# Kernel tuning notes

Hardware: AMD Instinct MI355X
Metric: run time of the kernel (lower is better)

Reference implementation:

```python
import jax, jax.numpy as jnp
from jax import lax
import numpy as np

VOCAB, EMB, HID, B, T = 500, 64, 64, 512, 512


def setup_inputs() -> dict:
    key = jax.random.key(0)
    ks = jax.random.split(key, 12)
    s_ih = 1.0 / np.sqrt(HID)
    emb = jax.random.normal(ks[0], (VOCAB, EMB), dtype=jnp.float32)
    emb = emb.at[0].set(0.0)  # padding_idx=0 row is zero-initialized
    u = lambda k, shape: jax.random.uniform(k, shape, jnp.float32, -s_ih, s_ih)
    return {
        "x": jax.random.randint(ks[1], (B, T), 0, VOCAB, dtype=jnp.int64),
        "emb": emb,
        "W_ih0": u(ks[2], (HID, EMB)), "W_hh0": u(ks[3], (HID, HID)),
        "b_ih0": u(ks[4], (HID,)),     "b_hh0": u(ks[5], (HID,)),
        "W_ih1": u(ks[6], (HID, HID)), "W_hh1": u(ks[7], (HID, HID)),
        "b_ih1": u(ks[8], (HID,)),     "b_hh1": u(ks[9], (HID,)),
        "fc_w": u(ks[10], (1, HID)),   "fc_b": u(ks[11], (1,)),
    }


def reference(x, emb, W_ih0, W_hh0, b_ih0, b_hh0, W_ih1, W_hh1, b_ih1, b_hh1, fc_w, fc_b):
    e = emb[x]                                        # [B,T,EMB]
    # Layer-0 input projection is time-parallel; precompute as one big GEMM.
    xin0 = jnp.einsum('bte,he->bth', e, W_ih0) + b_ih0  # [B,T,HID]

    def step(carry, xt):
        h1, h2 = carry
        h1 = jnp.tanh(xt + h1 @ W_hh0.T + b_hh0)
        h2 = jnp.tanh(h1 @ W_ih1.T + b_ih1 + h2 @ W_hh1.T + b_hh1)
        return (h1, h2), None

    h0 = jnp.zeros((x.shape[0], HID), dtype=e.dtype)
    (h1, h2), _ = lax.scan(step, (h0, h0), jnp.swapaxes(xin0, 0, 1))  # scan over T
    return h2 @ fc_w.T + fc_b                          # [B,1]
```

## Files before the change

### kernel.cpp

```cpp
#include <hip/hip_runtime.h>
#include <math.h>

#define VOCAB 500
#define EMB   64
#define HID   64
#define BB    512
#define TT    512
#define KC    8
#define NC    (TT / KC)

__device__ __forceinline__ float fast_tanh(float x) {
    float ax = fabsf(x);
    float e  = __expf(-2.0f * ax);
    float r  = __builtin_amdgcn_rcpf(1.0f + e);
    float t  = fmaf(-2.0f * e, r, 1.0f);
    return copysignf(t, x);
}

__device__ __forceinline__ float bcast(float v, int lane) {
    return __int_as_float(__builtin_amdgcn_readlane(__float_as_int(v), lane));
}

__global__ __launch_bounds__(64) void proj_kernel(
        const float* __restrict__ emb,
        const float* __restrict__ W_ih0,
        const float* __restrict__ b_ih0,
        float* __restrict__ proj) {
    const int v = blockIdx.x;
    const int j = threadIdx.x;
    const float4* e4 = (const float4*)(emb + v * EMB);
    const float4* w4 = (const float4*)(W_ih0 + j * EMB);
    float acc = b_ih0[j];
    #pragma unroll
    for (int k = 0; k < EMB / 4; ++k) {
        float4 e = e4[k];
        float4 w = w4[k];
        acc = fmaf(w.x, e.x, acc);
        acc = fmaf(w.y, e.y, acc);
        acc = fmaf(w.z, e.z, acc);
        acc = fmaf(w.w, e.w, acc);
    }
    proj[v * HID + j] = acc;
}

__global__ __launch_bounds__(192, 1) void rnn_kernel(
        const int*   __restrict__ x,
        const float* __restrict__ proj,
        const float* __restrict__ W_hh0,
        const float* __restrict__ b_hh0,
        const float* __restrict__ W_ih1,
        const float* __restrict__ W_hh1,
        const float* __restrict__ b_ih1,
        const float* __restrict__ b_hh1,
        const float* __restrict__ fc_w,
        const float* __restrict__ fc_b,
        float* __restrict__ out) {
    const int b   = blockIdx.x;
    const int tid = threadIdx.x;
    const int wid = tid >> 6;
    const int j   = tid & 63;

    __shared__ __align__(16) float H1R[2][KC][HID];
    __shared__ __align__(16) float AAR[2][KC][HID];
    __shared__ int xls[TT];

    for (int t = tid; t < TT; t += 192) xls[t] = x[b * TT + t];

    const float* wsrc = (wid == 0 ? W_hh0 : (wid == 1 ? W_ih1 : W_hh1)) + j * HID;
    float w[HID];
    {
        const float4* w4 = (const float4*)wsrc;
        #pragma unroll
        for (int k = 0; k < HID / 4; ++k) {
            float4 t4 = w4[k];
            w[4*k+0] = t4.x; w[4*k+1] = t4.y; w[4*k+2] = t4.z; w[4*k+3] = t4.w;
        }
    }
    #pragma unroll
    for (int k = 0; k < HID; ++k) asm volatile("" : "+v"(w[k]));

    const float bh0 = b_hh0[j];
    const float bi1 = b_ih1[j] + b_hh1[j];
    const float fcw = fc_w[j];

    __syncthreads();

    float h1reg = 0.0f, h2reg = 0.0f;
    float xin[KC], xinN[KC];
    if (wid == 0) {
        #pragma unroll
        for (int u = 0; u < KC; ++u) xin[u] = proj[xls[u] * HID + j];
    }

    for (int c = 0; c < NC + 2; ++c) {
        if (wid == 0) {
            if (c < NC) {
                const int base = ((c + 1) & (NC - 1)) * KC;
                #pragma unroll
                for (int u = 0; u < KC; ++u)
                    xinN[u] = proj[xls[base + u] * HID + j];

                #pragma unroll
                for (int u = 0; u < KC; ++u) {
                    float a0 = xin[u] + bh0, a1 = 0.0f, a2 = 0.0f, a3 = 0.0f;
                    #pragma unroll
                    for (int k = 0; k < HID; k += 4) {
                        a0 = fmaf(w[k+0], bcast(h1reg, k+0), a0);
                        a1 = fmaf(w[k+1], bcast(h1reg, k+1), a1);
                        a2 = fmaf(w[k+2], bcast(h1reg, k+2), a2);
                        a3 = fmaf(w[k+3], bcast(h1reg, k+3), a3);
                    }
                    h1reg = fast_tanh((a0 + a1) + (a2 + a3));
                    H1R[c & 1][u][j] = h1reg;
                    xin[u] = xinN[u];
                }
            }
        } else if (wid == 1) {
            if (c >= 1 && c <= NC) {
                const int p = (c - 1) & 1;
                #pragma unroll
                for (int u = 0; u < KC; ++u) {
                    const float4* hv = (const float4*)(&H1R[p][u][0]);
                    float a0 = 0.0f, a1 = 0.0f, a2 = 0.0f, a3 = 0.0f;
                    #pragma unroll
                    for (int k = 0; k < HID / 4; ++k) {
                        float4 h = hv[k];
                        a0 = fmaf(w[4*k+0], h.x, a0);
                        a1 = fmaf(w[4*k+1], h.y, a1);
                        a2 = fmaf(w[4*k+2], h.z, a2);
                        a3 = fmaf(w[4*k+3], h.w, a3);
                    }
                    AAR[p][u][j] = (a0 + a1) + (a2 + a3);
                }
            }
        } else {
            if (c >= 2) {
                const int p = c & 1;
                #pragma unroll
                for (int u = 0; u < KC; ++u) {
                    float a0 = AAR[p][u][j] + bi1, a1 = 0.0f, a2 = 0.0f, a3 = 0.0f;
                    #pragma unroll
                    for (int k = 0; k < HID; k += 4) {
                        a0 = fmaf(w[k+0], bcast(h2reg, k+0), a0);
                        a1 = fmaf(w[k+1], bcast(h2reg, k+1), a1);
                        a2 = fmaf(w[k+2], bcast(h2reg, k+2), a2);
                        a3 = fmaf(w[k+3], bcast(h2reg, k+3), a3);
                    }
                    h2reg = fast_tanh((a0 + a1) + (a2 + a3));
                }
            }
        }
        __syncthreads();
    }

    if (wid == 2) {
        float val = h2reg * fcw;
        #pragma unroll
        for (int o = 32; o > 0; o >>= 1) val += __shfl_down(val, o, 64);
        if (j == 0) out[b] = val + fc_b[0];
    }
}

extern "C" void kernel_launch(void* const* d_in, const int* in_sizes, int n_in,
                              void* d_out, int out_size, void* d_ws, size_t ws_size,
                              hipStream_t stream) {
    const int*   x     = (const int*)  d_in[0];
    const float* emb   = (const float*)d_in[1];
    const float* W_ih0 = (const float*)d_in[2];
    const float* W_hh0 = (const float*)d_in[3];
    const float* b_ih0 = (const float*)d_in[4];
    const float* b_hh0 = (const float*)d_in[5];
    const float* W_ih1 = (const float*)d_in[6];
    const float* W_hh1 = (const float*)d_in[7];
    const float* b_ih1 = (const float*)d_in[8];
    const float* b_hh1 = (const float*)d_in[9];
    const float* fc_w  = (const float*)d_in[10];
    const float* fc_b  = (const float*)d_in[11];
    float* out  = (float*)d_out;
    float* proj = (float*)d_ws;

    proj_kernel<<<VOCAB, 64, 0, stream>>>(emb, W_ih0, b_ih0, proj);
    rnn_kernel<<<BB, 192, 0, stream>>>(x, proj, W_hh0, b_hh0,
                                       W_ih1, W_hh1, b_ih1, b_hh1,
                                       fc_w, fc_b, out);
}
```

Baseline: 318.4 us.

## Process two batch rows per block to interleave independent recurrences

```diff
diff --git a/kernel.cpp b/kernel.cpp
--- a/kernel.cpp
+++ b/kernel.cpp
@@ -6,7 +6,8 @@
 #define HID   64
 #define BB    512
 #define TT    512
-#define KC    8
+#define RB    2
+#define KC    4
 #define NC    (TT / KC)
 
 __device__ __forceinline__ float fast_tanh(float x) {
@@ -55,16 +56,17 @@
         const float* __restrict__ fc_w,
         const float* __restrict__ fc_b,
         float* __restrict__ out) {
-    const int b   = blockIdx.x;
+    const int b0  = blockIdx.x * RB;
     const int tid = threadIdx.x;
     const int wid = tid >> 6;
     const int j   = tid & 63;
 
-    __shared__ __align__(16) float H1R[2][KC][HID];
-    __shared__ __align__(16) float AAR[2][KC][HID];
-    __shared__ int xls[TT];
-
-    for (int t = tid; t < TT; t += 192) xls[t] = x[b * TT + t];
+    __shared__ __align__(16) float H1R[2][KC][RB][HID];
+    __shared__ __align__(16) float AAR[2][KC][RB][HID];
+    __shared__ int xls[RB][TT];
+
+    for (int t = tid; t < RB * TT; t += 192)
+        ((int*)xls)[t] = x[b0 * TT + t];
 
     const float* wsrc = (wid == 0 ? W_hh0 : (wid == 1 ? W_ih1 : W_hh1)) + j * HID;
     float w[HID];
@@ -85,11 +87,14 @@
 
     __syncthreads();
 
-    float h1reg = 0.0f, h2reg = 0.0f;
-    float xin[KC], xinN[KC];
+    float h1A = 0.0f, h1B = 0.0f, h2A = 0.0f, h2B = 0.0f;
+    float xinA[KC], xinB[KC], xnA[KC], xnB[KC];
     if (wid == 0) {
         #pragma unroll
-        for (int u = 0; u < KC; ++u) xin[u] = proj[xls[u] * HID + j];
+        for (int u = 0; u < KC; ++u) {
+            xinA[u] = proj[xls[0][u] * HID + j];
+            xinB[u] = proj[xls[1][u] * HID + j];
+        }
     }
 
     for (int c = 0; c < NC + 2; ++c) {
@@ -97,22 +102,31 @@
             if (c < NC) {
                 const int base = ((c + 1) & (NC - 1)) * KC;
                 #pragma unroll
-                for (int u = 0; u < KC; ++u)
-                    xinN[u] = proj[xls[base + u] * HID + j];
-
-                #pragma unroll
-                for (int u = 0; u < KC; ++u) {
-                    float a0 = xin[u] + bh0, a1 = 0.0f, a2 = 0.0f, a3 = 0.0f;
+                for (int u = 0; u < KC; ++u) {
+                    xnA[u] = proj[xls[0][base + u] * HID + j];
+                    xnB[u] = proj[xls[1][base + u] * HID + j];
+                }
+                #pragma unroll
+                for (int u = 0; u < KC; ++u) {
+                    float aA0 = xinA[u] + bh0, aA1 = 0.0f, aA2 = 0.0f, aA3 = 0.0f;
+                    float aB0 = xinB[u] + bh0, aB1 = 0.0f, aB2 = 0.0f, aB3 = 0.0f;
                     #pragma unroll
                     for (int k = 0; k < HID; k += 4) {
-                        a0 = fmaf(w[k+0], bcast(h1reg, k+0), a0);
-                        a1 = fmaf(w[k+1], bcast(h1reg, k+1), a1);
-                        a2 = fmaf(w[k+2], bcast(h1reg, k+2), a2);
-                        a3 = fmaf(w[k+3], bcast(h1reg, k+3), a3);
+                        aA0 = fmaf(w[k+0], bcast(h1A, k+0), aA0);
+                        aB0 = fmaf(w[k+0], bcast(h1B, k+0), aB0);
+                        aA1 = fmaf(w[k+1], bcast(h1A, k+1), aA1);
+                        aB1 = fmaf(w[k+1], bcast(h1B, k+1), aB1);
+                        aA2 = fmaf(w[k+2], bcast(h1A, k+2), aA2);
+                        aB2 = fmaf(w[k+2], bcast(h1B, k+2), aB2);
+                        aA3 = fmaf(w[k+3], bcast(h1A, k+3), aA3);
+                        aB3 = fmaf(w[k+3], bcast(h1B, k+3), aB3);
                     }
-                    h1reg = fast_tanh((a0 + a1) + (a2 + a3));
-                    H1R[c & 1][u][j] = h1reg;
-                    xin[u] = xinN[u];
+                    h1A = fast_tanh((aA0 + aA1) + (aA2 + aA3));
+                    h1B = fast_tanh((aB0 + aB1) + (aB2 + aB3));
+                    H1R[c & 1][u][0][j] = h1A;
+                    H1R[c & 1][u][1][j] = h1B;
+                    xinA[u] = xnA[u];
+                    xinB[u] = xnB[u];
                 }
             }
         } else if (wid == 1) {
@@ -120,17 +134,23 @@
                 const int p = (c - 1) & 1;
                 #pragma unroll
                 for (int u = 0; u < KC; ++u) {
-                    const float4* hv = (const float4*)(&H1R[p][u][0]);
-                    float a0 = 0.0f, a1 = 0.0f, a2 = 0.0f, a3 = 0.0f;
+                    const float vA = H1R[p][u][0][j];
+                    const float vB = H1R[p][u][1][j];
+                    float aA0 = 0.0f, aA1 = 0.0f, aA2 = 0.0f, aA3 = 0.0f;
+                    float aB0 = 0.0f, aB1 = 0.0f, aB2 = 0.0f, aB3 = 0.0f;
                     #pragma unroll
-                    for (int k = 0; k < HID / 4; ++k) {
-                        float4 h = hv[k];
-                        a0 = fmaf(w[4*k+0], h.x, a0);
-                        a1 = fmaf(w[4*k+1], h.y, a1);
-                        a2 = fmaf(w[4*k+2], h.z, a2);
-                        a3 = fmaf(w[4*k+3], h.w, a3);
+                    for (int k = 0; k < HID; k += 4) {
+                        aA0 = fmaf(w[k+0], bcast(vA, k+0), aA0);
+                        aB0 = fmaf(w[k+0], bcast(vB, k+0), aB0);
+                        aA1 = fmaf(w[k+1], bcast(vA, k+1), aA1);
+                        aB1 = fmaf(w[k+1], bcast(vB, k+1), aB1);
+                        aA2 = fmaf(w[k+2], bcast(vA, k+2), aA2);
+                        aB2 = fmaf(w[k+2], bcast(vB, k+2), aB2);
+                        aA3 = fmaf(w[k+3], bcast(vA, k+3), aA3);
+                        aB3 = fmaf(w[k+3], bcast(vB, k+3), aB3);
                     }
-                    AAR[p][u][j] = (a0 + a1) + (a2 + a3);
+                    AAR[p][u][0][j] = (aA0 + aA1) + (aA2 + aA3);
+                    AAR[p][u][1][j] = (aB0 + aB1) + (aB2 + aB3);
                 }
             }
         } else {
@@ -138,15 +158,21 @@
                 const int p = c & 1;
                 #pragma unroll
                 for (int u = 0; u < KC; ++u) {
-                    float a0 = AAR[p][u][j] + bi1, a1 = 0.0f, a2 = 0.0f, a3 = 0.0f;
+                    float aA0 = AAR[p][u][0][j] + bi1, aA1 = 0.0f, aA2 = 0.0f, aA3 = 0.0f;
+                    float aB0 = AAR[p][u][1][j] + bi1, aB1 = 0.0f, aB2 = 0.0f, aB3 = 0.0f;
                     #pragma unroll
                     for (int k = 0; k < HID; k += 4) {
-                        a0 = fmaf(w[k+0], bcast(h2reg, k+0), a0);
-                        a1 = fmaf(w[k+1], bcast(h2reg, k+1), a1);
-                        a2 = fmaf(w[k+2], bcast(h2reg, k+2), a2);
-                        a3 = fmaf(w[k+3], bcast(h2reg, k+3), a3);
+                        aA0 = fmaf(w[k+0], bcast(h2A, k+0), aA0);
+                        aB0 = fmaf(w[k+0], bcast(h2B, k+0), aB0);
+                        aA1 = fmaf(w[k+1], bcast(h2A, k+1), aA1);
+                        aB1 = fmaf(w[k+1], bcast(h2B, k+1), aB1);
+                        aA2 = fmaf(w[k+2], bcast(h2A, k+2), aA2);
+                        aB2 = fmaf(w[k+2], bcast(h2B, k+2), aB2);
+                        aA3 = fmaf(w[k+3], bcast(h2A, k+3), aA3);
+                        aB3 = fmaf(w[k+3], bcast(h2B, k+3), aB3);
                     }
-                    h2reg = fast_tanh((a0 + a1) + (a2 + a3));
+                    h2A = fast_tanh((aA0 + aA1) + (aA2 + aA3));
+                    h2B = fast_tanh((aB0 + aB1) + (aB2 + aB3));
                 }
             }
         }
@@ -154,10 +180,17 @@
     }
 
     if (wid == 2) {
-        float val = h2reg * fcw;
+        float vA = h2A * fcw;
+        float vB = h2B * fcw;
         #pragma unroll
-        for (int o = 32; o > 0; o >>= 1) val += __shfl_down(val, o, 64);
-        if (j == 0) out[b] = val + fc_b[0];
+        for (int o = 32; o > 0; o >>= 1) {
+            vA += __shfl_down(vA, o, 64);
+            vB += __shfl_down(vB, o, 64);
+        }
+        if (j == 0) {
+            out[b0 + 0] = vA + fc_b[0];
+            out[b0 + 1] = vB + fc_b[0];
+        }
     }
 }
 
@@ -180,7 +213,7 @@
     float* proj = (float*)d_ws;
 
     proj_kernel<<<VOCAB, 64, 0, stream>>>(emb, W_ih0, b_ih0, proj);
-    rnn_kernel<<<BB, 192, 0, stream>>>(x, proj, W_hh0, b_hh0,
-                                       W_ih1, W_hh1, b_ih1, b_hh1,
-                                       fc_w, fc_b, out);
-}
+    rnn_kernel<<<BB / RB, 192, 0, stream>>>(x, proj, W_hh0, b_hh0,
+                                            W_ih1, W_hh1, b_ih1, b_hh1,
+                                            fc_w, fc_b, out);
+}
```

Result: slower. 553.3 us (+73.8%).
